# Kernel tuning notes

Hardware: AMD Instinct MI355X
Metric: run time of the kernel (lower is better)

The kernel has to match this reference:

```python
import jax, jax.numpy as jnp
import numpy as np

B, N, E = 32, 1024, 16384
IN_DIM, HID, OUT = 768, 512, 400
H, F = 2, 200          # gat heads, per-head dim (H*F == OUT)
PAIR = 2 * OUT         # 800
NEG_SLOPE = 0.2


def setup_inputs() -> dict:
    key = jax.random.key(0)
    ks = jax.random.split(key, 20)
    g = lambda k, shp, fan: jax.random.normal(k, shp, jnp.float32) * (1.0 / np.sqrt(fan))
    return {
        "patch_features": jax.random.normal(ks[0], (B, N, IN_DIM), jnp.float32),
        "edges": jax.random.randint(ks[1], (2, E), 0, N, jnp.int32),
        # patch_encoder Mlps: 768 -> 512 (GELU) -> 400
        "enc_w1": g(ks[2], (IN_DIM, HID), IN_DIM), "enc_b1": jnp.zeros((HID,), jnp.float32),
        "enc_w2": g(ks[3], (HID, OUT), HID),      "enc_b2": jnp.zeros((OUT,), jnp.float32),
        # single GATConv: 400 -> 2 heads x 200, concat
        "gat_w": g(ks[4], (OUT, H, F), OUT),
        "att_src": g(ks[5], (H, F), F), "att_dst": g(ks[6], (H, F), F),
        "gat_b": jnp.zeros((H * F,), jnp.float32),
        # predict_head Mlps: 800 -> 800 (GELU) -> 400 (GELU) -> 3
        "h_w1": g(ks[7], (PAIR, PAIR), PAIR),      "h_b1": jnp.zeros((PAIR,), jnp.float32),
        "h_w2": g(ks[8], (PAIR, PAIR // 2), PAIR), "h_b2": jnp.zeros((PAIR // 2,), jnp.float32),
        "h_w3": g(ks[9], (PAIR // 2, 3), PAIR // 2), "h_b3": jnp.zeros((3,), jnp.float32),
    }


def _forward(patch_features, edges, enc_w1, enc_b1, enc_w2, enc_b2,
             gat_w, att_src, att_dst, gat_b,
             h_w1, h_b1, h_w2, h_b2, h_w3, h_b3):
    n = patch_features.shape[1]
    # per-batch patch encoder MLP (dropout inactive at eval)
    enc = jax.nn.gelu(jnp.einsum('bni,ih->bnh', patch_features, enc_w1) + enc_b1)
    enc = jnp.einsum('bnh,ho->bno', enc, enc_w2) + enc_b2   # [B,N,400]

    src0, dst0 = edges[0], edges[1]
    # GATConv adds self-loops
    loops = jnp.arange(n, dtype=edges.dtype)
    src = jnp.concatenate([src0, loops])
    dst = jnp.concatenate([dst0, loops])

    def gat(h):                                   # h: [N,400]
        wh = jnp.einsum('no,ohf->nhf', h, gat_w)  # [N,H,F]
        a_s = jnp.sum(wh * att_src, -1)           # [N,H]
        a_d = jnp.sum(wh * att_dst, -1)
        e = a_s[src] + a_d[dst]                   # [Et,H]
        e = jnp.where(e > 0, e, NEG_SLOPE * e)    # LeakyReLU(0.2)
        m = jax.ops.segment_max(e, dst, num_segments=n)
        ee = jnp.exp(e - m[dst])
        z = jax.ops.segment_sum(ee, dst, num_segments=n)
        coef = ee / z[dst]                        # softmax over incoming edges
        out = jax.ops.segment_sum(coef[:, :, None] * wh[src], dst, num_segments=n)
        return out.reshape(n, H * F) + gat_b      # concat heads + bias

    feat = enc + jax.vmap(gat)(enc)               # residual add per batch

    # pairwise edge gather + predict head
    pair = jnp.concatenate([feat[:, src0], feat[:, dst0]], axis=-1)  # [B,E,800]
    p = jax.nn.gelu(jnp.einsum('bep,pq->beq', pair, h_w1) + h_b1)
    p = jax.nn.gelu(jnp.einsum('beq,qr->ber', p, h_w2) + h_b2)
    pred = jnp.einsum('ber,rs->bes', p, h_w3) + h_b3                 # [B,E,3]
    return feat, pred


def reference(patch_features, edges, enc_w1, enc_b1, enc_w2, enc_b2,
              gat_w, att_src, att_dst, gat_b,
              h_w1, h_b1, h_w2, h_b2, h_w3, h_b3):
    return _forward(patch_features, edges, enc_w1, enc_b1, enc_w2, enc_b2,
                    gat_w, att_src, att_dst, gat_b,
                    h_w1, h_b1, h_w2, h_b2, h_w3, h_b3)
```

## Files before the change

### kernel.cpp

```cpp
#include <hip/hip_runtime.h>
#include <hip/hip_bf16.h>

typedef unsigned short u16;
typedef __attribute__((ext_vector_type(8))) short bf16x8;
typedef __attribute__((ext_vector_type(4))) float f32x4;

#define B_   32
#define N_   1024
#define E_   16384
#define ET_  17408
#define IN_DIM 768
#define HID  512
#define OUT_ 400
#define PAIR_ 800
#define UVW_ 1600
#define FEAT_ELEMS 13107200
#define MAXD 128

__device__ __forceinline__ float u2f(u16 u) {
    union { unsigned int i; float f; } v; v.i = ((unsigned int)u) << 16; return v.f;
}
__device__ __forceinline__ u16 f2u(float f) {
    __hip_bfloat16 h = __float2bfloat16(f);
    return *(u16*)&h;
}
__device__ __forceinline__ unsigned int pack2(float a, float b) {
    return (unsigned int)f2u(a) | ((unsigned int)f2u(b) << 16);
}

__device__ __forceinline__ float gelu_f(float x) {
    const float c = 0.7978845608028654f;
    float u = c * (x + 0.044715f * x * x * x);
    float t = 2.0f / (1.0f + __expf(-2.0f * u)) - 1.0f;
    return 0.5f * x * (1.0f + t);
}

__device__ __forceinline__ void load_lds16(const void* g, void* l) {
    __builtin_amdgcn_global_load_lds(
        (const __attribute__((address_space(1))) void*)g,
        (__attribute__((address_space(3))) void*)l, 16, 0, 0);
}

__global__ void wt_k(const float* __restrict__ W, u16* __restrict__ Wt,
                     int K, int N)
{
    int i = blockIdx.x * 256 + threadIdx.x;
    if (i >= N * K) return;
    int n = i / K, k = i - n * K;
    Wt[i] = f2u(W[(size_t)k * N + n]);
}

__global__ void wtuv_k(const float* __restrict__ W, u16* __restrict__ Wt)
{
    int i = blockIdx.x * 256 + threadIdx.x;
    if (i >= UVW_ * OUT_) return;
    int n = i / OUT_, k = i - n * OUT_;
    int row = (n >= PAIR_) ? OUT_ + k : k;
    int col = (n >= PAIR_) ? n - PAIR_ : n;
    Wt[i] = f2u(W[(size_t)row * PAIR_ + col]);
}

__global__ void f2b_k(const float* __restrict__ X, u16* __restrict__ Y, int n8)
{
    int i = blockIdx.x * 256 + threadIdx.x;
    if (i >= n8) return;
    const float4* p = (const float4*)X + (size_t)i * 2;
    float4 a = p[0], b = p[1];
    uint4 o;
    o.x = pack2(a.x, a.y); o.y = pack2(a.z, a.w);
    o.z = pack2(b.x, b.y); o.w = pack2(b.z, b.w);
    ((uint4*)Y)[i] = o;
}

template<int ASRC, bool DO_GELU, bool HAS_BIAS, bool OUT_F32, bool FUSE_H3>
__global__ __launch_bounds__(256)
void mfma_gemm_k(const float* __restrict__ Af, const u16* __restrict__ Ab,
                 const u16* __restrict__ Wt, const float* __restrict__ bias,
                 u16* __restrict__ Cb, float* __restrict__ Cf,
                 int M, int N, int K,
                 const u16* __restrict__ zbuf,
                 const float* __restrict__ w3p, float* __restrict__ partp)
{
    __shared__ __align__(16) u16 As[128 * 64];
    __shared__ __align__(16) u16 Bs[128 * 64];
    const int tid  = threadIdx.x;
    const int gx   = gridDim.x;
    const int nwg  = gx * gridDim.y;
    const int orig = blockIdx.y * gx + blockIdx.x;
    const int qc   = nwg >> 3, rc = nwg & 7;
    const int xcd  = orig & 7, lid = orig >> 3;
    const int wg   = ((xcd < rc) ? xcd * (qc + 1) : rc * (qc + 1) + (xcd - rc) * qc) + lid;
    const int bnIdx= wg % gx;
    const int bm   = (wg / gx) * 128;
    const int bn   = bnIdx * 128;
    const int wave = tid >> 6;
    const int lane = tid & 63;
    const int wm   = (wave >> 1) * 64;
    const int wn   = (wave & 1) * 64;
    const int lm   = lane & 15;
    const int lq   = lane >> 4;
    const int lb   = lm & 7;
    const int l8 = lane >> 3;
    const int cl = (lane & 7) ^ l8;

    size_t arow[4]; size_t brow[4]; bool bok[4];
    #pragma unroll
    for (int c4 = 0; c4 < 4; ++c4) {
        int rt = wave * 32 + c4 * 8 + l8;
        if (ASRC == 1) arow[c4] = (size_t)(bm + rt) * K;
        int n = bn + rt;
        bok[c4] = (n < N);
        brow[c4] = (size_t)(n < N ? n : 0) * K;
    }
    const int vrow = tid >> 1, vhalf = tid & 1;

    f32x4 acc[4][4] = {};

    for (int k0 = 0; k0 < K; k0 += 64) {
        if (ASRC == 1) {
            int kk = k0 + cl * 8;
            #pragma unroll
            for (int c4 = 0; c4 < 4; ++c4) {
                const u16* ga = (kk < K) ? Ab + arow[c4] + kk : zbuf;
                load_lds16(ga, (char*)As + (wave * 32 + c4 * 8) * 128);
            }
        } else {
            #pragma unroll
            for (int c = 0; c < 4; ++c) {
                int c_log = vhalf * 4 + c;
                int kk = k0 + c_log * 8;
                uint4 wv = make_uint4(0, 0, 0, 0);
                if (kk < K) {
                    const float* p = Af + (size_t)(bm + vrow) * K + kk;
                    float4 v0 = *(const float4*)p;
                    float4 v1 = *(const float4*)(p + 4);
                    wv.x = pack2(v0.x, v0.y); wv.y = pack2(v0.z, v0.w);
                    wv.z = pack2(v1.x, v1.y); wv.w = pack2(v1.z, v1.w);
                }
                int pc = c_log ^ (vrow & 7);
                *(uint4*)((char*)As + vrow * 128 + pc * 16) = wv;
            }
        }
        {
            int kk = k0 + cl * 8;
            #pragma unroll
            for (int c4 = 0; c4 < 4; ++c4) {
                const u16* gb = (bok[c4] && kk < K) ? Wt + brow[c4] + kk : zbuf;
                load_lds16(gb, (char*)Bs + (wave * 32 + c4 * 8) * 128);
            }
        }
        __syncthreads();
        #pragma unroll
        for (int kh = 0; kh < 2; ++kh) {
            bf16x8 af[4], bfr[4];
            #pragma unroll
            for (int t = 0; t < 4; ++t)
                af[t] = *(const bf16x8*)((const char*)As +
                        (wm + t * 16 + lm) * 128 + (((kh * 4 + lq) ^ lb) * 16));
            #pragma unroll
            for (int u = 0; u < 4; ++u)
                bfr[u] = *(const bf16x8*)((const char*)Bs +
                        (wn + u * 16 + lm) * 128 + (((kh * 4 + lq) ^ lb) * 16));
            #pragma unroll
            for (int t = 0; t < 4; ++t)
                #pragma unroll
                for (int u = 0; u < 4; ++u)
                    acc[t][u] = __builtin_amdgcn_mfma_f32_16x16x32_bf16(
                        af[t], bfr[u], acc[t][u], 0, 0, 0);
        }
        __syncthreads();
    }

    if (FUSE_H3) {
        float w3c[4][3]; float bvv[4];
        #pragma unroll
        for (int u = 0; u < 4; ++u) {
            int col = bn + wn + u * 16 + lm;
            bool ok = (col < N);
            bvv[u]    = ok ? bias[col] : 0.f;
            w3c[u][0] = ok ? w3p[col * 3 + 0] : 0.f;
            w3c[u][1] = ok ? w3p[col * 3 + 1] : 0.f;
            w3c[u][2] = ok ? w3p[col * 3 + 2] : 0.f;
        }
        float* red = (float*)As;
        #pragma unroll
        for (int t = 0; t < 4; ++t) {
            #pragma unroll
            for (int r = 0; r < 4; ++r) {
                float s0 = 0.f, s1 = 0.f, s2 = 0.f;
                #pragma unroll
                for (int u = 0; u < 4; ++u) {
                    float v = gelu_f(acc[t][u][r] + bvv[u]);
                    s0 += v * w3c[u][0];
                    s1 += v * w3c[u][1];
                    s2 += v * w3c[u][2];
                }
                #pragma unroll
                for (int off = 8; off; off >>= 1) {
                    s0 += __shfl_xor(s0, off);
                    s1 += __shfl_xor(s1, off);
                    s2 += __shfl_xor(s2, off);
                }
                if (lm == 0) {
                    int lr = t * 16 + lq * 4 + r;
                    float* d = red + (wave * 64 + lr) * 3;
                    d[0] = s0; d[1] = s1; d[2] = s2;
                }
            }
        }
        __syncthreads();
        if ((wave & 1) == 0 && lane < 64) {
            int lr = lane;
            int rowg = bm + wm + lr;
            float* a = red + ((wave + 0) * 64 + lr) * 3;
            float* b = red + ((wave + 1) * 64 + lr) * 3;
            float* d = partp + ((size_t)bnIdx * M + rowg) * 3;
            d[0] = a[0] + b[0];
            d[1] = a[1] + b[1];
            d[2] = a[2] + b[2];
        }
        return;
    }

    #pragma unroll
    for (int u = 0; u < 4; ++u) {
        int col = bn + wn + u * 16 + lm;
        if (col >= N) continue;
        float bv = HAS_BIAS ? bias[col] : 0.f;
        #pragma unroll
        for (int t = 0; t < 4; ++t) {
            #pragma unroll
            for (int r = 0; r < 4; ++r) {
                int rowg = bm + wm + t * 16 + lq * 4 + r;
                float v = acc[t][u][r] + bv;
                if (DO_GELU) v = gelu_f(v);
                if (OUT_F32) {
                    Cf[(size_t)rowg * N + col] = v;
                    if (Cb) Cb[(size_t)rowg * N + col] = f2u(v);
                } else {
                    Cb[(size_t)rowg * N + col] = f2u(v);
                }
            }
        }
    }
}

__global__ __launch_bounds__(256)
void red3_k(const float* __restrict__ part, const float* __restrict__ b3,
            float* __restrict__ out, int row_base, int Mr)
{
    int r = blockIdx.x * 256 + threadIdx.x;
    if (r >= Mr) return;
    float s0 = b3[0], s1 = b3[1], s2 = b3[2];
    #pragma unroll
    for (int s = 0; s < 4; ++s) {
        const float* p = part + ((size_t)s * Mr + r) * 3;
        s0 += p[0]; s1 += p[1]; s2 += p[2];
    }
    float* d = out + (size_t)FEAT_ELEMS + (size_t)(row_base + r) * 3;
    d[0] = s0; d[1] = s1; d[2] = s2;
}

__global__ __launch_bounds__(256)
void pair_fuse_k(const u16* __restrict__ UV, const float* __restrict__ b1,
                 const int* __restrict__ src0, const int* __restrict__ dst0,
                 u16* __restrict__ p1, int b0, int nrows)
{
    unsigned idx = blockIdx.x * 256u + threadIdx.x;
    unsigned total = (unsigned)nrows * 100u;
    if (idx >= total) return;
    unsigned r  = (unsigned)(((unsigned long long)idx * 1374389535ull) >> 37);
    unsigned c8 = idx - r * 100u;
    int e = r & (E_ - 1);
    int gs, gd;
    if (b0 >= 0) {
        int b = b0 + (int)(r >> 14);
        gs = (b << 10) + src0[e];
        gd = (b << 10) + dst0[e];
    } else {
        gs = src0[e]; gd = dst0[e];
    }
    uint4 qu = *(const uint4*)(UV + (size_t)gs * UVW_ + c8 * 8);
    uint4 qv = *(const uint4*)(UV + (size_t)gd * UVW_ + PAIR_ + c8 * 8);
    float4 bva = *(const float4*)(b1 + c8 * 8);
    float4 bvb = *(const float4*)(b1 + c8 * 8 + 4);
    float bb[8] = {bva.x, bva.y, bva.z, bva.w, bvb.x, bvb.y, bvb.z, bvb.w};
    unsigned int uu[4] = {qu.x, qu.y, qu.z, qu.w};
    unsigned int vv[4] = {qv.x, qv.y, qv.z, qv.w};
    uint4 o; unsigned int* op = (unsigned int*)&o;
    #pragma unroll
    for (int q = 0; q < 4; ++q) {
        float a0 = u2f((u16)(uu[q] & 0xffff)) + u2f((u16)(vv[q] & 0xffff)) + bb[2*q];
        float a1 = u2f((u16)(uu[q] >> 16))    + u2f((u16)(vv[q] >> 16))    + bb[2*q+1];
        op[q] = pack2(gelu_f(a0), gelu_f(a1));
    }
    *(uint4*)(p1 + (size_t)r * PAIR_ + c8 * 8) = o;
}

__global__ __launch_bounds__(256)
void scores_k(const u16* __restrict__ wh, const float* __restrict__ att_s,
              const float* __restrict__ att_d, float* __restrict__ a_s,
              float* __restrict__ a_d)
{
    int n = blockIdx.x * 4 + (threadIdx.x >> 6);
    int lane = threadIdx.x & 63;
    const u16* row = wh + (size_t)n * OUT_;
    float as0 = 0, as1 = 0, ad0 = 0, ad1 = 0;
    for (int f = lane; f < OUT_; f += 64) {
        float v = u2f(row[f]);
        float s = att_s[f];
        float d = att_d[f];
        if (f < 200) { as0 += v * s; ad0 += v * d; }
        else         { as1 += v * s; ad1 += v * d; }
    }
    for (int off = 32; off; off >>= 1) {
        as0 += __shfl_xor(as0, off); as1 += __shfl_xor(as1, off);
        ad0 += __shfl_xor(ad0, off); ad1 += __shfl_xor(ad1, off);
    }
    if (lane == 0) {
        a_s[(size_t)n * 2 + 0] = as0; a_s[(size_t)n * 2 + 1] = as1;
        a_d[(size_t)n * 2 + 0] = ad0; a_d[(size_t)n * 2 + 1] = ad1;
    }
}

__global__ void csr_count_k(const int* __restrict__ edges, int* __restrict__ deg)
{
    int et = blockIdx.x * blockDim.x + threadIdx.x;
    if (et >= ET_) return;
    int dst = (et < E_) ? edges[E_ + et] : (et - E_);
    atomicAdd(&deg[dst], 1);
}

__global__ __launch_bounds__(1024)
void csr_scan_k(const int* __restrict__ deg, int* __restrict__ row_ptr,
                int* __restrict__ cnt)
{
    __shared__ int s[1024];
    int t = threadIdx.x;
    int d = deg[t];
    s[t] = d;
    __syncthreads();
    for (int off = 1; off < 1024; off <<= 1) {
        int v = (t >= off) ? s[t - off] : 0;
        __syncthreads();
        s[t] += v;
        __syncthreads();
    }
    row_ptr[t] = s[t] - d;
    cnt[t] = s[t] - d;
    if (t == 1023) row_ptr[1024] = s[t];
}

__global__ void csr_fill_k(const int* __restrict__ edges, int* __restrict__ cnt,
                           int* __restrict__ col_src)
{
    int et = blockIdx.x * blockDim.x + threadIdx.x;
    if (et >= ET_) return;
    int src, dst;
    if (et < E_) { src = edges[et]; dst = edges[E_ + et]; }
    else         { src = et - E_;  dst = src; }
    int pos = atomicAdd(&cnt[dst], 1);
    col_src[pos] = src;
}

__global__ __launch_bounds__(256)
void gat_k(const u16* __restrict__ wh,
           const float* __restrict__ a_s, const float* __restrict__ a_d,
           const int* __restrict__ row_ptr, const int* __restrict__ col_src,
           const float* __restrict__ gat_b, float* __restrict__ feat,
           u16* __restrict__ featb16)
{
    int gn = blockIdx.x;
    int b = gn >> 10, n = gn & 1023;
    int tid = threadIdx.x;
    __shared__ float s_ee[2][MAXD];
    __shared__ int   s_src[MAXD];
    __shared__ float s_misc[6];
    __shared__ float s_part[4][50][9];
    int start = row_ptr[n];
    int deg = row_ptr[n + 1] - start;

    if (tid < 64) {
        int lane = tid;
        float ad0 = a_d[(size_t)gn * 2 + 0];
        float ad1 = a_d[(size_t)gn * 2 + 1];
        float m0 = -1e30f, m1 = -1e30f;
        for (int j = lane; j < deg; j += 64) {
            int gs = (b << 10) + col_src[start + j];
            float e0 = a_s[(size_t)gs * 2 + 0] + ad0; e0 = (e0 > 0.f) ? e0 : 0.2f * e0;
            float e1 = a_s[(size_t)gs * 2 + 1] + ad1; e1 = (e1 > 0.f) ? e1 : 0.2f * e1;
            if (j < MAXD) { s_ee[0][j] = e0; s_ee[1][j] = e1; s_src[j] = gs; }
            m0 = fmaxf(m0, e0); m1 = fmaxf(m1, e1);
        }
        for (int off = 32; off; off >>= 1) {
            m0 = fmaxf(m0, __shfl_xor(m0, off));
            m1 = fmaxf(m1, __shfl_xor(m1, off));
        }
        float z0 = 0.f, z1 = 0.f;
        for (int j = lane; j < deg; j += 64) {
            float e0, e1;
            if (j < MAXD) { e0 = s_ee[0][j]; e1 = s_ee[1][j]; }
            else {
                int gs = (b << 10) + col_src[start + j];
                e0 = a_s[(size_t)gs * 2 + 0] + ad0; e0 = (e0 > 0.f) ? e0 : 0.2f * e0;
                e1 = a_s[(size_t)gs * 2 + 1] + ad1; e1 = (e1 > 0.f) ? e1 : 0.2f * e1;
            }
            float t0 = __expf(e0 - m0), t1 = __expf(e1 - m1);
            if (j < MAXD) { s_ee[0][j] = t0; s_ee[1][j] = t1; }
            z0 += t0; z1 += t1;
        }
        for (int off = 32; off; off >>= 1) {
            z0 += __shfl_xor(z0, off);
            z1 += __shfl_xor(z1, off);
        }
        if (lane == 0) {
            s_misc[0] = m0; s_misc[1] = m1;
            s_misc[2] = (z0 > 0.f) ? 1.f / z0 : 0.f;
            s_misc[3] = (z1 > 0.f) ? 1.f / z1 : 0.f;
            s_misc[4] = ad0; s_misc[5] = ad1;
        }
    }
    __syncthreads();

    int wv = tid >> 6, ln = tid & 63;
    if (ln < 50) {
        int h = (ln >= 25);
        float m = s_misc[h], ad = s_misc[4 + h];
        float acc[8] = {};
        for (int j = wv; j < deg; j += 4) {
            float w; int gs;
            if (j < MAXD) { w = s_ee[h][j]; gs = s_src[j]; }
            else {
                gs = (b << 10) + col_src[start + j];
                float e = a_s[(size_t)gs * 2 + h] + ad;
                e = (e > 0.f) ? e : 0.2f * e;
                w = __expf(e - m);
            }
            uint4 q = *(const uint4*)(wh + (size_t)gs * OUT_ + ln * 8);
            acc[0] += w * u2f((u16)(q.x & 0xffff));
            acc[1] += w * u2f((u16)(q.x >> 16));
            acc[2] += w * u2f((u16)(q.y & 0xffff));
            acc[3] += w * u2f((u16)(q.y >> 16));
            acc[4] += w * u2f((u16)(q.z & 0xffff));
            acc[5] += w * u2f((u16)(q.z >> 16));
            acc[6] += w * u2f((u16)(q.w & 0xffff));
            acc[7] += w * u2f((u16)(q.w >> 16));
        }
        #pragma unroll
        for (int k = 0; k < 8; ++k) s_part[wv][ln][k] = acc[k];
    }
    __syncthreads();
    if (tid < 50) {
        int h = (tid >= 25);
        float iz = s_misc[2 + h];
        size_t base = (size_t)gn * OUT_ + tid * 8;
        float4 f0 = *(const float4*)(feat + base);
        float4 f1 = *(const float4*)(feat + base + 4);
        float fv[8] = { f0.x, f0.y, f0.z, f0.w, f1.x, f1.y, f1.z, f1.w };
        float o[8];
        #pragma unroll
        for (int k = 0; k < 8; ++k) {
            float s = s_part[0][tid][k] + s_part[1][tid][k] +
                      s_part[2][tid][k] + s_part[3][tid][k];
            o[k] = fv[k] + s * iz + gat_b[tid * 8 + k];
        }
        *(float4*)(feat + base)     = make_float4(o[0], o[1], o[2], o[3]);
        *(float4*)(feat + base + 4) = make_float4(o[4], o[5], o[6], o[7]);
        if (featb16) {
            uint4 bq;
            bq.x = pack2(o[0], o[1]); bq.y = pack2(o[2], o[3]);
            bq.z = pack2(o[4], o[5]); bq.w = pack2(o[6], o[7]);
            *(uint4*)(featb16 + base) = bq;
        }
    }
}

__global__ __launch_bounds__(256)
void head3_k(const u16* __restrict__ p2, const float* __restrict__ w3,
             const float* __restrict__ b3, float* __restrict__ out,
             int row_base, int nrows)
{
    int wv = threadIdx.x >> 6, lane = threadIdx.x & 63;
    float w3r[24];
    if (lane < 50) {
        #pragma unroll
        for (int q = 0; q < 6; ++q) {
            float4 v = *(const float4*)(w3 + lane * 24 + q * 4);
            w3r[q * 4 + 0] = v.x; w3r[q * 4 + 1] = v.y;
            w3r[q * 4 + 2] = v.z; w3r[q * 4 + 3] = v.w;
        }
    }
    int e0 = blockIdx.x * 16 + wv * 4;
    for (int ei = 0; ei < 4; ++ei) {
        int e = e0 + ei;
        if (e >= nrows) break;
        float s0 = 0, s1 = 0, s2 = 0;
        if (lane < 50) {
            uint4 q = *(const uint4*)(p2 + (size_t)e * OUT_ + lane * 8);
            float f[8];
            f[0] = u2f((u16)(q.x & 0xffff)); f[1] = u2f((u16)(q.x >> 16));
            f[2] = u2f((u16)(q.y & 0xffff)); f[3] = u2f((u16)(q.y >> 16));
            f[4] = u2f((u16)(q.z & 0xffff)); f[5] = u2f((u16)(q.z >> 16));
            f[6] = u2f((u16)(q.w & 0xffff)); f[7] = u2f((u16)(q.w >> 16));
            #pragma unroll
            for (int k = 0; k < 8; ++k) {
                s0 += f[k] * w3r[k * 3 + 0];
                s1 += f[k] * w3r[k * 3 + 1];
                s2 += f[k] * w3r[k * 3 + 2];
            }
        }
        for (int off = 32; off; off >>= 1) {
            s0 += __shfl_xor(s0, off);
            s1 += __shfl_xor(s1, off);
            s2 += __shfl_xor(s2, off);
        }
        if (lane == 0) {
            size_t o = (size_t)FEAT_ELEMS + (size_t)(row_base + e) * 3;
            out[o + 0] = s0 + b3[0];
            out[o + 1] = s1 + b3[1];
            out[o + 2] = s2 + b3[2];
        }
    }
}

extern "C" void kernel_launch(void* const* d_in, const int* in_sizes, int n_in,
                              void* d_out, int out_size, void* d_ws, size_t ws_size,
                              hipStream_t stream)
{
    const float* patch  = (const float*)d_in[0];
    const int*   edges  = (const int*)d_in[1];
    const float* enc_w1 = (const float*)d_in[2];
    const float* enc_b1 = (const float*)d_in[3];
    const float* enc_w2 = (const float*)d_in[4];
    const float* enc_b2 = (const float*)d_in[5];
    const float* gat_w  = (const float*)d_in[6];
    const float* att_s  = (const float*)d_in[7];
    const float* att_d  = (const float*)d_in[8];
    const float* gat_b  = (const float*)d_in[9];
    const float* h_w1   = (const float*)d_in[10];
    const float* h_b1   = (const float*)d_in[11];
    const float* h_w2   = (const float*)d_in[12];
    const float* h_b2   = (const float*)d_in[13];
    const float* h_w3   = (const float*)d_in[14];
    const float* h_b3   = (const float*)d_in[15];
    float* out  = (float*)d_out;
    float* feat = out;
    char*  ws   = (char*)d_ws;

    const int* src0 = edges;
    const int* dst0 = edges + E_;

    const size_t R0 = 33554432ull, TAIL = 4194304ull;
    const size_t UVSZ = 104857600ull;
    const size_t P1SZ = 26214400ull;
    int CB = 0;
    if      (ws_size >= R0 + UVSZ + TAIL + 4 * P1SZ) CB = 4;
    else if (ws_size >= R0 + UVSZ + TAIL + 2 * P1SZ) CB = 2;
    const bool big = (CB >= 2);

    u16 *enc1, *whb, *p1, *p2, *featb16, *uv, *w1t, *w2t, *gwt, *uvwt, *hw2t;
    u16 *patchb16, *encb16;
    float *a_s, *a_d, *part; int *deg;
    if (big) {
        enc1    = (u16*)ws;
        featb16 = (u16*)ws;
        part    = (float*)ws;
        whb     = (u16*)(ws + R0);
        uv      = (u16*)(ws + R0);
        encb16  = (u16*)(ws + R0 + 26214400ull);
        p1      = (u16*)(ws + R0 + UVSZ);
        patchb16= (u16*)(ws + R0 + UVSZ);
        p2      = nullptr;
        size_t tb = (ws_size - TAIL) & ~(size_t)255;
        w1t  = (u16*)(ws + tb);
        w2t  = (u16*)(ws + tb + 786432);
        gwt  = (u16*)(ws + tb + 1196032);
        uvwt = (u16*)(ws + tb + 1516032);
        hw2t = (u16*)(ws + tb + 2796032);
        a_s  = (float*)(ws + tb + 3436032);
        a_d  = (float*)(ws + tb + 3698176);
        deg  = (int*)(ws + tb + 3960320);
    } else {
        enc1    = (u16*)ws;
        whb     = (u16*)ws;
        p1      = (u16*)ws;
        featb16 = nullptr;
        patchb16= nullptr;
        encb16  = nullptr;
        part    = nullptr;
        p2      = (u16*)(ws + 26214400);
        uv      = (u16*)(ws + 39321600);
        w1t  = (u16*)(ws + 42598400);
        w2t  = (u16*)(ws + 43384832);
        gwt  = (u16*)(ws + 43794432);
        uvwt = (u16*)(ws + 44114432);
        hw2t = (u16*)(ws + 45394432);
        a_s  = (float*)(ws + 46034432);
        a_d  = (float*)(ws + 46296576);
        deg  = (int*)(ws + 46558720);
    }
    int* row_ptr = deg + 1024;
    int* cnt     = row_ptr + 1032;
    int* col_src = cnt + 1024;
    u16* zbuf = (u16*)(col_src + 17408);

    hipMemsetAsync(zbuf, 0, 256, stream);

    wt_k<<<(HID * IN_DIM + 255) / 256, 256, 0, stream>>>(enc_w1, w1t, IN_DIM, HID);
    wt_k<<<(OUT_ * HID + 255) / 256, 256, 0, stream>>>(enc_w2, w2t, HID, OUT_);
    wt_k<<<(OUT_ * OUT_ + 255) / 256, 256, 0, stream>>>(gat_w, gwt, OUT_, OUT_);
    wtuv_k<<<(UVW_ * OUT_ + 255) / 256, 256, 0, stream>>>(h_w1, uvwt);
    wt_k<<<(OUT_ * PAIR_ + 255) / 256, 256, 0, stream>>>(h_w2, hw2t, PAIR_, OUT_);

    hipMemsetAsync(deg, 0, 1024 * sizeof(int), stream);
    csr_count_k<<<(ET_ + 255) / 256, 256, 0, stream>>>(edges, deg);
    csr_scan_k<<<1, 1024, 0, stream>>>(deg, row_ptr, cnt);
    csr_fill_k<<<(ET_ + 255) / 256, 256, 0, stream>>>(edges, cnt, col_src);

    if (big) {
        f2b_k<<<(B_ * N_ * IN_DIM / 8 + 255) / 256, 256, 0, stream>>>(
            patch, patchb16, B_ * N_ * IN_DIM / 8);
        mfma_gemm_k<1, true, true, false, false><<<dim3(HID / 128, (B_ * N_) / 128), 256, 0, stream>>>(
            nullptr, patchb16, w1t, enc_b1, enc1, nullptr, B_ * N_, HID, IN_DIM, zbuf,
            nullptr, nullptr);
        mfma_gemm_k<1, false, true, true, false><<<dim3((OUT_ + 127) / 128, (B_ * N_) / 128), 256, 0, stream>>>(
            nullptr, enc1, w2t, enc_b2, encb16, feat, B_ * N_, OUT_, HID, zbuf,
            nullptr, nullptr);
        mfma_gemm_k<1, false, false, false, false><<<dim3((OUT_ + 127) / 128, (B_ * N_) / 128), 256, 0, stream>>>(
            nullptr, encb16, gwt, nullptr, whb, nullptr, B_ * N_, OUT_, OUT_, zbuf,
            nullptr, nullptr);
    } else {
        mfma_gemm_k<0, true, true, false, false><<<dim3(HID / 128, (B_ * N_) / 128), 256, 0, stream>>>(
            patch, nullptr, w1t, enc_b1, enc1, nullptr, B_ * N_, HID, IN_DIM, zbuf,
            nullptr, nullptr);
        mfma_gemm_k<1, false, true, true, false><<<dim3((OUT_ + 127) / 128, (B_ * N_) / 128), 256, 0, stream>>>(
            nullptr, enc1, w2t, enc_b2, nullptr, feat, B_ * N_, OUT_, HID, zbuf,
            nullptr, nullptr);
        mfma_gemm_k<0, false, false, false, false><<<dim3((OUT_ + 127) / 128, (B_ * N_) / 128), 256, 0, stream>>>(
            feat, nullptr, gwt, nullptr, whb, nullptr, B_ * N_, OUT_, OUT_, zbuf,
            nullptr, nullptr);
    }

    scores_k<<<(B_ * N_) / 4, 256, 0, stream>>>(whb, att_s, att_d, a_s, a_d);
    gat_k<<<B_ * N_, 256, 0, stream>>>(whb, a_s, a_d, row_ptr, col_src,
                                       gat_b, feat, featb16);

    if (big) {
        mfma_gemm_k<1, false, false, false, false><<<dim3((UVW_ + 127) / 128, (B_ * N_) / 128), 256, 0, stream>>>(
            nullptr, featb16, uvwt, nullptr, uv, nullptr, B_ * N_, UVW_, OUT_, zbuf,
            nullptr, nullptr);
        for (int b0 = 0; b0 < B_; b0 += CB) {
            int Mr = CB * E_;
            pair_fuse_k<<<(Mr * 100 + 255) / 256, 256, 0, stream>>>(
                uv, h_b1, src0, dst0, p1, b0, Mr);
            mfma_gemm_k<1, true, true, false, true><<<dim3((OUT_ + 127) / 128, Mr / 128), 256, 0, stream>>>(
                nullptr, p1, hw2t, h_b2, nullptr, nullptr, Mr, OUT_, PAIR_, zbuf,
                h_w3, part);
            red3_k<<<(Mr + 255) / 256, 256, 0, stream>>>(part, h_b3, out, b0 * E_, Mr);
        }
    } else {
        for (int b = 0; b < B_; ++b) {
            const float* featb = feat + (size_t)b * N_ * OUT_;
            mfma_gemm_k<0, false, false, false, false><<<dim3((UVW_ + 127) / 128, N_ / 128), 256, 0, stream>>>(
                featb, nullptr, uvwt, nullptr, uv, nullptr, N_, UVW_, OUT_, zbuf,
                nullptr, nullptr);
            pair_fuse_k<<<(E_ * 100 + 255) / 256, 256, 0, stream>>>(
                uv, h_b1, src0, dst0, p1, -1, E_);
            mfma_gemm_k<1, true, true, false, false><<<dim3((OUT_ + 127) / 128, E_ / 128), 256, 0, stream>>>(
                nullptr, p1, hw2t, h_b2, p2, nullptr, E_, OUT_, PAIR_, zbuf,
                nullptr, nullptr);
            head3_k<<<(E_ + 15) / 16, 256, 0, stream>>>(p2, h_w3, h_b3, out,
                                                        b * E_, E_);
        }
    }
}
```

Measured before the change: 1.647 ms.

## Double-buffer LDS tiles in bf16-A GEMM path to overlap loads with MFMA

For the GEMM variant whose A operand is already bf16 (direct-to-LDS loads), the A and B tiles are now double-buffered in shared memory. The next K tile is prefetched while MFMAs run on the current one, with explicit vmcnt waits and raw barriers replacing the two __syncthreads per iteration. This doubles LDS use per block to 64KB, which may reduce occupancy, and relies on hand-counted vmcnt values staying correct.

```diff
diff --git a/kernel.cpp b/kernel.cpp
--- a/kernel.cpp
+++ b/kernel.cpp
@@ -81,8 +81,8 @@
                  const u16* __restrict__ zbuf,
                  const float* __restrict__ w3p, float* __restrict__ partp)
 {
-    __shared__ __align__(16) u16 As[128 * 64];
-    __shared__ __align__(16) u16 Bs[128 * 64];
+    __shared__ __align__(16) u16 As[2][128 * 64];
+    __shared__ __align__(16) u16 Bs[2][128 * 64];
     const int tid  = threadIdx.x;
     const int gx   = gridDim.x;
     const int nwg  = gx * gridDim.y;
@@ -115,16 +115,56 @@
     const int vrow = tid >> 1, vhalf = tid & 1;
 
     f32x4 acc[4][4] = {};
-
-    for (int k0 = 0; k0 < K; k0 += 64) {
-        if (ASRC == 1) {
+    const int NT = (K + 63) >> 6;
+
+    if (ASRC == 1) {
+        auto stage = [&](int buf, int k0) {
             int kk = k0 + cl * 8;
             #pragma unroll
             for (int c4 = 0; c4 < 4; ++c4) {
                 const u16* ga = (kk < K) ? Ab + arow[c4] + kk : zbuf;
-                load_lds16(ga, (char*)As + (wave * 32 + c4 * 8) * 128);
-            }
-        } else {
+                load_lds16(ga, (char*)As[buf] + (wave * 32 + c4 * 8) * 128);
+            }
+            #pragma unroll
+            for (int c4 = 0; c4 < 4; ++c4) {
+                const u16* gb = (bok[c4] && kk < K) ? Wt + brow[c4] + kk : zbuf;
+                load_lds16(gb, (char*)Bs[buf] + (wave * 32 + c4 * 8) * 128);
+            }
+        };
+        stage(0, 0);
+        int cur = 0;
+        for (int it = 0; it < NT; ++it) {
+            const bool last = (it == NT - 1);
+            if (!last) stage(cur ^ 1, (it + 1) * 64);
+            if (!last) asm volatile("s_waitcnt vmcnt(8)" ::: "memory");
+            else       asm volatile("s_waitcnt vmcnt(0)" ::: "memory");
+            __builtin_amdgcn_s_barrier();
+            const char* Abase = (const char*)As[cur];
+            const char* Bbase = (const char*)Bs[cur];
+            #pragma unroll
+            for (int kh = 0; kh < 2; ++kh) {
+                bf16x8 af[4], bfr[4];
+                #pragma unroll
+                for (int t = 0; t < 4; ++t)
+                    af[t] = *(const bf16x8*)(Abase +
+                            (wm + t * 16 + lm) * 128 + (((kh * 4 + lq) ^ lb) * 16));
+                #pragma unroll
+                for (int u = 0; u < 4; ++u)
+                    bfr[u] = *(const bf16x8*)(Bbase +
+                            (wn + u * 16 + lm) * 128 + (((kh * 4 + lq) ^ lb) * 16));
+                #pragma unroll
+                for (int t = 0; t < 4; ++t)
+                    #pragma unroll
+                    for (int u = 0; u < 4; ++u)
+                        acc[t][u] = __builtin_amdgcn_mfma_f32_16x16x32_bf16(
+                            af[t], bfr[u], acc[t][u], 0, 0, 0);
+            }
+            asm volatile("" ::: "memory");
+            __builtin_amdgcn_s_barrier();
+            cur ^= 1;
+        }
+    } else {
+        for (int k0 = 0; k0 < K; k0 += 64) {
             #pragma unroll
             for (int c = 0; c < 4; ++c) {
                 int c_log = vhalf * 4 + c;
@@ -138,37 +178,37 @@
                     wv.z = pack2(v1.x, v1.y); wv.w = pack2(v1.z, v1.w);
                 }
                 int pc = c_log ^ (vrow & 7);
-                *(uint4*)((char*)As + vrow * 128 + pc * 16) = wv;
-            }
-        }
-        {
-            int kk = k0 + cl * 8;
+                *(uint4*)((char*)As[0] + vrow * 128 + pc * 16) = wv;
+            }
+            {
+                int kk = k0 + cl * 8;
+                #pragma unroll
+                for (int c4 = 0; c4 < 4; ++c4) {
+                    const u16* gb = (bok[c4] && kk < K) ? Wt + brow[c4] + kk : zbuf;
+                    load_lds16(gb, (char*)Bs[0] + (wave * 32 + c4 * 8) * 128);
+                }
+            }
+            __syncthreads();
             #pragma unroll
-            for (int c4 = 0; c4 < 4; ++c4) {
-                const u16* gb = (bok[c4] && kk < K) ? Wt + brow[c4] + kk : zbuf;
-                load_lds16(gb, (char*)Bs + (wave * 32 + c4 * 8) * 128);
-            }
-        }
-        __syncthreads();
-        #pragma unroll
-        for (int kh = 0; kh < 2; ++kh) {
-            bf16x8 af[4], bfr[4];
-            #pragma unroll
-            for (int t = 0; t < 4; ++t)
-                af[t] = *(const bf16x8*)((const char*)As +
-                        (wm + t * 16 + lm) * 128 + (((kh * 4 + lq) ^ lb) * 16));
-            #pragma unroll
-            for (int u = 0; u < 4; ++u)
-                bfr[u] = *(const bf16x8*)((const char*)Bs +
-                        (wn + u * 16 + lm) * 128 + (((kh * 4 + lq) ^ lb) * 16));
-            #pragma unroll
-            for (int t = 0; t < 4; ++t)
+            for (int kh = 0; kh < 2; ++kh) {
+                bf16x8 af[4], bfr[4];
+                #pragma unroll
+                for (int t = 0; t < 4; ++t)
+                    af[t] = *(const bf16x8*)((const char*)As[0] +
+                            (wm + t * 16 + lm) * 128 + (((kh * 4 + lq) ^ lb) * 16));
                 #pragma unroll
                 for (int u = 0; u < 4; ++u)
-                    acc[t][u] = __builtin_amdgcn_mfma_f32_16x16x32_bf16(
-                        af[t], bfr[u], acc[t][u], 0, 0, 0);
-        }
-        __syncthreads();
+                    bfr[u] = *(const bf16x8*)((const char*)Bs[0] +
+                            (wn + u * 16 + lm) * 128 + (((kh * 4 + lq) ^ lb) * 16));
+                #pragma unroll
+                for (int t = 0; t < 4; ++t)
+                    #pragma unroll
+                    for (int u = 0; u < 4; ++u)
+                        acc[t][u] = __builtin_amdgcn_mfma_f32_16x16x32_bf16(
+                            af[t], bfr[u], acc[t][u], 0, 0, 0);
+            }
+            __syncthreads();
+        }
     }
 
     if (FUSE_H3) {
```

After: 1.631 ms. Within noise of the previous version (-0.9%).
